# Optimization experiments

Hardware: AMD Instinct MI355X
Metric: run time of the kernel (lower is better)

The kernel has to match this reference:

```python
import jax, jax.numpy as jnp
import numpy as np
from jax import lax

# ---- static config (from cfg) ----
B, NCLS, CREG, H, W = 16, 3, 50, 96, 320
K = 100                  # DETECTIONS_PER_IMG
DOWN = 4                 # BACKBONE.DOWN_RATIO
THRESH = 0.2             # DETECTIONS_THRESHOLD
IMG_W, IMG_H = W * DOWN, H * DOWN
EPS = 1e-6
# channel layout in pred_reg (kvper):
#  0:4 dim_2d | 4:6 offset_3d | 6:9 dim_3d | 9:25 orient | 25:45 corner_offset
#  45:48 corner_uncertainty | 48 depth | 49 depth_uncertainty


def setup_inputs() -> dict:
    key = jax.random.key(0)
    k1, k2, k3 = jax.random.split(key, 3)
    # shift heatmap logits negative so only a sparse set passes the threshold
    pred_hmp = jax.random.normal(k1, (B, NCLS, H, W), jnp.float32) * 2.0 - 2.0
    pred_reg = jax.random.normal(k2, (B, CREG, H, W), jnp.float32) * 0.5
    # KITTI P2 intrinsics: [f_u, c_u, f_v, c_v] per image
    calib = jnp.tile(jnp.array([[721.5377, 609.5593, 721.5377, 172.854]],
                               jnp.float32), (B, 1))
    pad_size = jnp.zeros((B, 2), jnp.float32)
    # per-class mean dims (l, h, w): Car / Pedestrian / Cyclist
    dim_mean = jnp.array([[3.88, 1.53, 1.63],
                          [0.84, 1.76, 0.66],
                          [1.76, 1.73, 0.60]], jnp.float32)
    return {"pred_hmp": pred_hmp, "pred_reg": pred_reg, "calib": calib,
            "pad_size": pad_size, "dim_mean": dim_mean}


def reference(pred_hmp, pred_reg, calib, pad_size, dim_mean):
    f32 = pred_hmp.dtype
    # ---- nms_hm: sigmoid + 3x3 max-pool suppression ----
    heat = jax.nn.sigmoid(pred_hmp)
    hmax = lax.reduce_window(heat, -jnp.inf, lax.max,
                             (1, 1, 3, 3), (1, 1, 1, 1), 'SAME')
    heat = jnp.where(hmax == heat, heat, jnp.zeros((), f32))
    # ---- select_topk (CenterNet-style): per-class topk then global topk ----
    flat = heat.reshape(B, NCLS, H * W)
    s1, i1 = lax.top_k(flat, K)                        # (B, C, K)
    s2, i2 = lax.top_k(s1.reshape(B, NCLS * K), K)     # (B, K)
    classes = i2 // K                                  # (B, K)
    inds = jnp.take_along_axis(i1.reshape(B, NCLS * K), i2, axis=1)  # flat h*w idx
    ys = (inds // W).astype(f32)
    xs = (inds % W).astype(f32)
    # ---- select_point_of_interest: gather 50-ch reg features at topk points ----
    regf = pred_reg.transpose(0, 2, 3, 1).reshape(B, H * W, CREG)
    pois = jnp.take_along_axis(regf, inds[:, :, None], axis=1).reshape(B * K, CREG)

    scores = s2.reshape(-1)                            # (N,) N = B*K
    cls = classes.reshape(-1)
    pts = jnp.stack([xs.reshape(-1), ys.reshape(-1)], axis=1)  # (N, 2)
    mask = (scores >= THRESH).astype(f32)
    bidx = jnp.repeat(jnp.arange(B), K)                # per-detection batch index

    reg2d = jax.nn.relu(pois[:, 0:4])                  # l, t, r, b
    off3d = pois[:, 4:6]
    dimoff = pois[:, 6:9]
    kpt = pois[:, 25:45].reshape(-1, 10, 2)            # 10 keypoints (x, y)
    cunc = jnp.exp(pois[:, 45:48])                     # corner uncertainty
    doff = pois[:, 48]
    dunc = jnp.exp(pois[:, 49:50])                     # direct depth uncertainty

    # ---- decode_dim3d: exp offset scaled by class mean dims ----
    dims = jnp.exp(dimoff) * dim_mean[cls]             # (N, 3); dims[:,1] = height
    h3d = dims[:, 1]

    # ---- decode_depth (inv_sigmoid) ----
    direct_depth = jnp.clip(1.0 / jax.nn.sigmoid(doff) - 1.0, 0.1, 100.0)

    # ---- decode_depth_from_kpts_batch: pinhole height -> depth ----
    fu = calib[bidx, 0]; cu = calib[bidx, 1]
    fv = calib[bidx, 2]; cv = calib[bidx, 3]
    ctr_h = kpt[:, 8, 1] - kpt[:, 9, 1]                       # bottom - top center
    c02_h = kpt[:, jnp.array([0, 2]), 1] - kpt[:, jnp.array([4, 6]), 1]
    c13_h = kpt[:, jnp.array([1, 3]), 1] - kpt[:, jnp.array([5, 7]), 1]
    d_ctr = fu * h3d / (jax.nn.relu(ctr_h) * DOWN + EPS)
    d_02 = ((fu * h3d)[:, None] / (jax.nn.relu(c02_h) * DOWN + EPS)).mean(axis=1)
    d_13 = ((fu * h3d)[:, None] / (jax.nn.relu(c13_h) * DOWN + EPS)).mean(axis=1)
    kpt_depths = jnp.clip(jnp.stack([d_ctr, d_02, d_13], axis=1), 0.1, 100.0)

    # ---- 'soft' depth ensemble: uncertainty-weighted average ----
    comb_d = jnp.concatenate([direct_depth[:, None], kpt_depths], axis=1)  # (N,4)
    comb_u = jnp.concatenate([dunc, cunc], axis=1)                          # (N,4)
    wts = 1.0 / comb_u
    wts = wts / wts.sum(axis=1, keepdims=True)
    depth = (comb_d * wts).sum(axis=1)
    depth_err = (wts * comb_u).sum(axis=1)

    # ---- decode_box2d_fcos ----
    pad = pad_size[bidx]                               # (N, 2)
    box2d = jnp.concatenate([pts - reg2d[:, :2], pts + reg2d[:, 2:]],
                            axis=1) * DOWN - jnp.tile(pad, (1, 2))
    hi = jnp.array([IMG_W - 1, IMG_H - 1, IMG_W - 1, IMG_H - 1], f32)
    box2d = jnp.clip(box2d, 0.0, hi)

    # ---- decode_loc3d: unproject projected 3D center at estimated depth ----
    proj = (pts + off3d) * DOWN - pad                  # (N, 2) image-plane uv
    x3 = (proj[:, 0] - cu) * depth / fu
    y3 = (proj[:, 1] - cv) * depth / fv
    loc3d = jnp.stack([x3, y3, depth], axis=1)

    result = jnp.concatenate([cls.astype(f32)[:, None], scores[:, None],
                              box2d, dims, loc3d, depth_err[:, None]], axis=1)
    return result * mask[:, None]                      # (B*K, 13)
```

## Files before the change

kernel.cpp:

```cpp
#include <hip/hip_runtime.h>
#include <math.h>


#define W_ 320
#define H_ 96
#define HW_ (W_ * H_)
#define LDSW 322
#define LDSH 98
#define CANDCAP 4096
#define BITS_02 0x3E4CCCCDu

__global__ __launch_bounds__(1024) void nms_topk(
    const float* __restrict__ hmp,
    unsigned long long* __restrict__ s1) {
  const int plane = blockIdx.x;
  const int t = threadIdx.x;
  const float* p = hmp + (size_t)plane * HW_;

  __shared__ float lp[LDSH * LDSW];
  __shared__ unsigned cand[CANDCAP];
  __shared__ unsigned long long skey[1024];
  __shared__ int hist[1024];
  __shared__ int part[1024];
  __shared__ int cnt, mcnt, cutbin;

  if (t == 0) { cnt = 0; mcnt = 0; cutbin = 0; }
  hist[t] = 0;
  for (int i = t; i < LDSH * LDSW; i += 1024) lp[i] = -INFINITY;
  __syncthreads();

  const float4* p4 = (const float4*)p;
  for (int i = t; i < HW_ / 4; i += 1024) {
    float4 v = p4[i];
    int gi0 = i * 4;
    int row = gi0 / W_;
    int col = gi0 - row * W_;
    float* d = &lp[(row + 1) * LDSW + col + 1];
    d[0] = v.x; d[1] = v.y; d[2] = v.z; d[3] = v.w;
  }
  __syncthreads();

  for (int i = t; i < HW_; i += 1024) {
    int row = i / W_;
    int col = i - row * W_;
    const float* c0 = &lp[row * LDSW + col];
    const float* c1 = &lp[(row + 1) * LDSW + col];
    const float* c2 = &lp[(row + 2) * LDSW + col];
    float v = c1[1];
    bool m = (v >= c0[0]) && (v >= c0[1]) && (v >= c0[2]) &&
             (v >= c1[0]) && (v >= c1[2]) &&
             (v >= c2[0]) && (v >= c2[1]) && (v >= c2[2]);
    if (m) {
      float s = 1.0f / (1.0f + expf(-v));
      if (s >= 0.2f) {
        unsigned bits = __float_as_uint(s);
        unsigned bin = (bits - BITS_02) >> 15;
        if (bin > 1023u) bin = 1023u;
        atomicAdd(&hist[bin], 1);
        int q = atomicAdd(&cnt, 1);
        if (q < CANDCAP) cand[q] = (unsigned)i;
      }
    }
  }
  __syncthreads();

  part[t] = hist[t];
  __syncthreads();
  for (int off = 1; off < 1024; off <<= 1) {
    int add = (t + off < 1024) ? part[t + off] : 0;
    __syncthreads();
    part[t] += add;
    __syncthreads();
  }
  if (part[t] >= 100 && (t == 1023 || part[t + 1] < 100)) cutbin = t;
  __syncthreads();
  const int cb = cutbin;
  const int n = min(cnt, CANDCAP);

  for (int i = t; i < n; i += 1024) {
    unsigned gi = cand[i];
    int row = (int)gi / W_;
    int col = (int)gi - row * W_;
    float v = lp[(row + 1) * LDSW + col + 1];
    float s = 1.0f / (1.0f + expf(-v));
    unsigned bits = __float_as_uint(s);
    unsigned bin = (bits - BITS_02) >> 15;
    if (bin > 1023u) bin = 1023u;
    if ((int)bin >= cb) {
      int q = atomicAdd(&mcnt, 1);
      if (q < 1024)
        skey[q] = ((unsigned long long)bits << 32) |
                  (unsigned long long)(0xFFFFFFFFu - gi);
    }
  }
  __syncthreads();
  const int m = min(mcnt, 1024);
  if (t >= m) skey[t] = 0ULL;
  __syncthreads();

  for (int k = 2; k <= 1024; k <<= 1) {
    for (int j = k >> 1; j > 0; j >>= 1) {
      int l = t ^ j;
      if (l > t) {
        unsigned long long a = skey[t], b2 = skey[l];
        if ((a > b2) == ((t & k) != 0)) { skey[t] = b2; skey[l] = a; }
      }
      __syncthreads();
    }
  }
  if (t < 100) s1[plane * 100 + t] = skey[t];
}

__global__ __launch_bounds__(256) void merge_decode(
    const unsigned long long* __restrict__ s1,
    const float* __restrict__ reg,
    const float* __restrict__ calib,
    const float* __restrict__ pad_size,
    const float* __restrict__ dim_mean,
    float* __restrict__ out) {
  const int b = blockIdx.x;
  const int t = threadIdx.x;

  __shared__ unsigned long long topk[300];
  __shared__ unsigned long long keys[512];
  __shared__ int selgi[100];
  __shared__ int selcls[100];
  __shared__ float selsc[100];
  __shared__ float pbuf[100 * 51];

  for (int i = t; i < 300; i += 256) topk[i] = s1[b * 300 + i];
  __syncthreads();
  for (int i = t; i < 512; i += 256) {
    unsigned long long kk = 0ULL;
    if (i < 300) {
      unsigned bits = (unsigned)(topk[i] >> 32);
      if (bits != 0u)
        kk = ((unsigned long long)bits << 32) |
             (unsigned long long)(0xFFFFFFFFu - (unsigned)i);
    }
    keys[i] = kk;
  }
  __syncthreads();
  for (int k = 2; k <= 512; k <<= 1) {
    for (int j = k >> 1; j > 0; j >>= 1) {
      for (int i = t; i < 512; i += 256) {
        int l = i ^ j;
        if (l > i) {
          unsigned long long a = keys[i], b2 = keys[l];
          if ((a > b2) == ((i & k) != 0)) { keys[i] = b2; keys[l] = a; }
        }
      }
      __syncthreads();
    }
  }

  if (t < 100) {
    unsigned long long key = keys[t];
    float score = __uint_as_float((unsigned)(key >> 32));
    if (score >= 0.2f) {
      unsigned pos = 0xFFFFFFFFu - (unsigned)(key & 0xFFFFFFFFull);
      selcls[t] = (int)(pos / 100u);
      unsigned long long e = topk[pos];
      selgi[t] = (int)(0xFFFFFFFFu - (unsigned)(e & 0xFFFFFFFFull));
      selsc[t] = score;
    } else {
      selgi[t] = -1;
      selcls[t] = 0;
      selsc[t] = 0.0f;
    }
  }
  __syncthreads();

  const float* rbase = reg + (size_t)b * 50 * HW_;
  for (int i = t; i < 100 * 50; i += 256) {
    int row = i % 100;
    int ch = i / 100;
    int gi = selgi[row];
    float v = 0.0f;
    if (gi >= 0) v = rbase[(size_t)ch * HW_ + gi];
    pbuf[row * 51 + ch] = v;
  }
  __syncthreads();

  if (t < 100) {
    float* orow = out + ((size_t)b * 100 + t) * 13;
    int gi = selgi[t];
    if (gi < 0) {
      #pragma unroll
      for (int i = 0; i < 13; ++i) orow[i] = 0.0f;
    } else {
      const float* p = &pbuf[t * 51];
      int cls = selcls[t];
      float score = selsc[t];
      int yy = gi / W_;
      int xx = gi - yy * W_;
      float x = (float)xx, y = (float)yy;

      float fu = calib[b * 4 + 0], cu = calib[b * 4 + 1];
      float fv = calib[b * 4 + 2], cv = calib[b * 4 + 3];
      float pad0 = pad_size[b * 2 + 0], pad1 = pad_size[b * 2 + 1];

      float r0 = fmaxf(p[0], 0.f), r1 = fmaxf(p[1], 0.f);
      float r2 = fmaxf(p[2], 0.f), r3 = fmaxf(p[3], 0.f);
      float bx0 = fminf(fmaxf((x - r0) * 4.f - pad0, 0.f), 1279.f);
      float by0 = fminf(fmaxf((y - r1) * 4.f - pad1, 0.f), 383.f);
      float bx1 = fminf(fmaxf((x + r2) * 4.f - pad0, 0.f), 1279.f);
      float by1 = fminf(fmaxf((y + r3) * 4.f - pad1, 0.f), 383.f);

      float d0 = expf(p[6]) * dim_mean[cls * 3 + 0];
      float d1 = expf(p[7]) * dim_mean[cls * 3 + 1];
      float d2 = expf(p[8]) * dim_mean[cls * 3 + 2];
      float h3d = d1;

      float sig = 1.0f / (1.0f + expf(-p[48]));
      float ddepth = fminf(fmaxf(1.0f / sig - 1.0f, 0.1f), 100.0f);

      float fh = fu * h3d;
      float d_ctr = fh / (fmaxf(p[42] - p[44], 0.f) * 4.f + 1e-6f);
      float d02 = 0.5f * (fh / (fmaxf(p[26] - p[34], 0.f) * 4.f + 1e-6f) +
                          fh / (fmaxf(p[30] - p[38], 0.f) * 4.f + 1e-6f));
      float d13 = 0.5f * (fh / (fmaxf(p[28] - p[36], 0.f) * 4.f + 1e-6f) +
                          fh / (fmaxf(p[32] - p[40], 0.f) * 4.f + 1e-6f));
      float kd0 = fminf(fmaxf(d_ctr, 0.1f), 100.f);
      float kd1 = fminf(fmaxf(d02, 0.1f), 100.f);
      float kd2 = fminf(fmaxf(d13, 0.1f), 100.f);

      float u0 = expf(p[49]), u1 = expf(p[45]), u2 = expf(p[46]), u3 = expf(p[47]);
      float w0 = 1.f / u0, w1 = 1.f / u1, w2 = 1.f / u2, w3 = 1.f / u3;
      float S = w0 + w1 + w2 + w3;
      float depth = (ddepth * w0 + kd0 * w1 + kd1 * w2 + kd2 * w3) / S;
      float derr = (w0 * u0 + w1 * u1 + w2 * u2 + w3 * u3) / S;

      float px = (x + p[4]) * 4.f - pad0;
      float py = (y + p[5]) * 4.f - pad1;
      float x3 = (px - cu) * depth / fu;
      float y3 = (py - cv) * depth / fv;

      orow[0] = (float)cls;
      orow[1] = score;
      orow[2] = bx0; orow[3] = by0; orow[4] = bx1; orow[5] = by1;
      orow[6] = d0;  orow[7] = d1;  orow[8] = d2;
      orow[9] = x3;  orow[10] = y3; orow[11] = depth;
      orow[12] = derr;
    }
  }
}

extern "C" void kernel_launch(void* const* d_in, const int* in_sizes, int n_in,
                              void* d_out, int out_size, void* d_ws, size_t ws_size,
                              hipStream_t stream) {
  const float* hmp   = (const float*)d_in[0];
  const float* reg   = (const float*)d_in[1];
  const float* calib = (const float*)d_in[2];
  const float* pads  = (const float*)d_in[3];
  const float* dm    = (const float*)d_in[4];
  float* out = (float*)d_out;

  unsigned long long* s1 = (unsigned long long*)d_ws;

  nms_topk<<<dim3(48), dim3(1024), 0, stream>>>(hmp, s1);
  merge_decode<<<dim3(16), dim3(256), 0, stream>>>(s1, reg, calib, pads, dm, out);
}
```

Measured before the change: 193.7 us.

## Vectorize NMS scan, wave-aggregate atomics, shrink scan and sort, batch gathers

The heatmap NMS pass now handles four pixels per thread from float2 LDS windows. It adds a logit pre-threshold, so sigmoid is skipped for values that cannot pass 0.2. Candidate appends use wave ballot and prefix ranks, so each wave does one atomic per batch instead of one per pixel. Only the LDS halo border is initialised to -inf, the histogram suffix scan becomes a single-wave shuffle scan, and the bitonic sort runs on 256 keys when few candidates survive. In merge_decode the 50-channel gathers are issued as 20 independent loads before the LDS stores, to raise memory-level parallelism at some register cost.

```diff
diff --git a/kernel.cpp b/kernel.cpp
--- a/kernel.cpp
+++ b/kernel.cpp
@@ -15,24 +15,31 @@
     unsigned long long* __restrict__ s1) {
   const int plane = blockIdx.x;
   const int t = threadIdx.x;
+  const int lane = t & 63;
   const float* p = hmp + (size_t)plane * HW_;
 
   __shared__ float lp[LDSH * LDSW];
   __shared__ unsigned cand[CANDCAP];
   __shared__ unsigned long long skey[1024];
   __shared__ int hist[1024];
-  __shared__ int part[1024];
   __shared__ int cnt, mcnt, cutbin;
 
   if (t == 0) { cnt = 0; mcnt = 0; cutbin = 0; }
   hist[t] = 0;
-  for (int i = t; i < LDSH * LDSW; i += 1024) lp[i] = -INFINITY;
-  __syncthreads();
+
+  if (t < 836) {
+    int idx;
+    if (t < 322)      idx = t;
+    else if (t < 644) idx = 97 * LDSW + (t - 322);
+    else if (t < 740) idx = (t - 644 + 1) * LDSW;
+    else              idx = (t - 740 + 1) * LDSW + 321;
+    lp[idx] = -INFINITY;
+  }
 
   const float4* p4 = (const float4*)p;
   for (int i = t; i < HW_ / 4; i += 1024) {
     float4 v = p4[i];
-    int gi0 = i * 4;
+    int gi0 = i << 2;
     int row = gi0 / W_;
     int col = gi0 - row * W_;
     float* d = &lp[(row + 1) * LDSW + col + 1];
@@ -40,39 +47,71 @@
   }
   __syncthreads();
 
-  for (int i = t; i < HW_; i += 1024) {
-    int row = i / W_;
-    int col = i - row * W_;
-    const float* c0 = &lp[row * LDSW + col];
-    const float* c1 = &lp[(row + 1) * LDSW + col];
-    const float* c2 = &lp[(row + 2) * LDSW + col];
-    float v = c1[1];
-    bool m = (v >= c0[0]) && (v >= c0[1]) && (v >= c0[2]) &&
-             (v >= c1[0]) && (v >= c1[2]) &&
-             (v >= c2[0]) && (v >= c2[1]) && (v >= c2[2]);
-    if (m) {
-      float s = 1.0f / (1.0f + expf(-v));
-      if (s >= 0.2f) {
-        unsigned bits = __float_as_uint(s);
-        unsigned bin = (bits - BITS_02) >> 15;
-        if (bin > 1023u) bin = 1023u;
-        atomicAdd(&hist[bin], 1);
-        int q = atomicAdd(&cnt, 1);
-        if (q < CANDCAP) cand[q] = (unsigned)i;
-      }
-    }
-  }
-  __syncthreads();
-
-  part[t] = hist[t];
-  __syncthreads();
-  for (int off = 1; off < 1024; off <<= 1) {
-    int add = (t + off < 1024) ? part[t + off] : 0;
-    __syncthreads();
-    part[t] += add;
-    __syncthreads();
-  }
-  if (part[t] >= 100 && (t == 1023 || part[t + 1] < 100)) cutbin = t;
+  for (int i = t; i < HW_ / 4; i += 1024) {
+    int r = i / 80;
+    int c4 = (i - r * 80) << 2;
+    const float2* w0 = (const float2*)&lp[r * LDSW + c4];
+    const float2* w1 = (const float2*)&lp[(r + 1) * LDSW + c4];
+    const float2* w2 = (const float2*)&lp[(r + 2) * LDSW + c4];
+    float2 a0 = w0[0], a1 = w0[1], a2 = w0[2];
+    float2 b0 = w1[0], b1 = w1[1], b2 = w1[2];
+    float2 e0 = w2[0], e1 = w2[1], e2 = w2[2];
+    float t0[6] = {a0.x, a0.y, a1.x, a1.y, a2.x, a2.y};
+    float t1[6] = {b0.x, b0.y, b1.x, b1.y, b2.x, b2.y};
+    float t2[6] = {e0.x, e0.y, e1.x, e1.y, e2.x, e2.y};
+    #pragma unroll
+    for (int j = 0; j < 4; ++j) {
+      float v = t1[j + 1];
+      bool pass = (v >= -1.3865f) &&
+                  (v >= t0[j]) && (v >= t0[j + 1]) && (v >= t0[j + 2]) &&
+                  (v >= t1[j]) && (v >= t1[j + 2]) &&
+                  (v >= t2[j]) && (v >= t2[j + 1]) && (v >= t2[j + 2]);
+      if (pass) {
+        float s = 1.0f / (1.0f + expf(-v));
+        pass = (s >= 0.2f);
+        if (pass) {
+          unsigned bits = __float_as_uint(s);
+          unsigned bin = (bits - BITS_02) >> 15;
+          if (bin > 1023u) bin = 1023u;
+          atomicAdd(&hist[bin], 1);
+        }
+      }
+      unsigned long long act = __ballot(pass);
+      if (pass) {
+        unsigned gi = (unsigned)(r * W_ + c4 + j);
+        int rank = __popcll(act & ((1ull << lane) - 1));
+        int base;
+        if (rank == 0) base = atomicAdd(&cnt, (int)__popcll(act));
+        base = __shfl(base, (int)__ffsll(act) - 1);
+        int q = base + rank;
+        if (q < CANDCAP) cand[q] = gi;
+      }
+    }
+  }
+  __syncthreads();
+
+  if (t < 64) {
+    int ssum = 0;
+    #pragma unroll
+    for (int k2 = 0; k2 < 16; ++k2) ssum += hist[t * 16 + k2];
+    int suf = ssum;
+    #pragma unroll
+    for (int off = 1; off < 64; off <<= 1) {
+      int o = __shfl_down(suf, off);
+      if (lane + off < 64) suf += o;
+    }
+    int sufn = __shfl_down(suf, 1);
+    if (lane == 63) sufn = 0;
+    if (suf >= 100 && sufn < 100) {
+      int acc = sufn;
+      int cb = t * 16;
+      for (int k2 = t * 16 + 15; k2 >= t * 16; --k2) {
+        acc += hist[k2];
+        if (acc >= 100) { cb = k2; break; }
+      }
+      cutbin = cb;
+    }
+  }
   __syncthreads();
   const int cb = cutbin;
   const int n = min(cnt, CANDCAP);
@@ -95,15 +134,18 @@
   }
   __syncthreads();
   const int m = min(mcnt, 1024);
-  if (t >= m) skey[t] = 0ULL;
-  __syncthreads();
-
-  for (int k = 2; k <= 1024; k <<= 1) {
+  const int N = (m <= 256) ? 256 : 1024;
+  if (t < N && t >= m) skey[t] = 0ULL;
+  __syncthreads();
+
+  for (int k = 2; k <= N; k <<= 1) {
     for (int j = k >> 1; j > 0; j >>= 1) {
-      int l = t ^ j;
-      if (l > t) {
-        unsigned long long a = skey[t], b2 = skey[l];
-        if ((a > b2) == ((t & k) != 0)) { skey[t] = b2; skey[l] = a; }
+      if (t < N) {
+        int l = t ^ j;
+        if (l > t) {
+          unsigned long long a = skey[t], b2 = skey[l];
+          if ((a > b2) == ((t & k) != 0)) { skey[t] = b2; skey[l] = a; }
+        }
       }
       __syncthreads();
     }
@@ -172,13 +214,22 @@
   __syncthreads();
 
   const float* rbase = reg + (size_t)b * 50 * HW_;
-  for (int i = t; i < 100 * 50; i += 256) {
-    int row = i % 100;
-    int ch = i / 100;
+  float gv[20];
+  int gidx[20];
+  #pragma unroll
+  for (int rr = 0; rr < 20; ++rr) {
+    int idx = rr * 256 + t;
+    bool ok = idx < 5000;
+    int row = ok ? (idx % 100) : 0;
+    int ch  = ok ? (idx / 100) : 0;
     int gi = selgi[row];
-    float v = 0.0f;
-    if (gi >= 0) v = rbase[(size_t)ch * HW_ + gi];
-    pbuf[row * 51 + ch] = v;
+    gv[rr] = (ok && gi >= 0) ? rbase[(size_t)ch * HW_ + gi] : 0.0f;
+    gidx[rr] = row * 51 + ch;
+  }
+  #pragma unroll
+  for (int rr = 0; rr < 20; ++rr) {
+    int idx = rr * 256 + t;
+    if (idx < 5000) pbuf[gidx[rr]] = gv[rr];
   }
   __syncthreads();
 
```

After: 186.1 us. 3.9% less time.
